# Kernel tuning notes

Measured on AMD Instinct MI355X. Metric: run time of the kernel, lower is better.

The kernel has to match this reference:

```python
import jax, jax.numpy as jnp
import numpy as np
from functools import partial

DN = ('NHWC', 'HWIO', 'NHWC')

def conv2d(x, w, stride=1, padding='SAME'):
    return jax.lax.conv_general_dilated(x, w, (stride, stride), padding, dimension_numbers=DN)

def hard_sigmoid(x):
    return jnp.clip(0.2 * x + 0.5, 0.0, 1.0)

def leaky_relu(x):
    return jnp.where(x >= 0, x, 0.3 * x)  # Keras LeakyReLU default alpha=0.3

def conv_lstm2d(inp, wx, wh, b):
    # inp: [B,T,H,W,Cin]; returns last hidden state h: [B,H,W,1]
    B, T, H, W, _ = inp.shape
    nf = wh.shape[2]  # filters = 1
    x_t_first = jnp.transpose(inp, (1, 0, 2, 3, 4))  # [T,B,H,W,Cin]
    h0 = jnp.zeros((B, H, W, nf), inp.dtype)
    c0 = jnp.zeros((B, H, W, nf), inp.dtype)

    def step(carry, x_t):
        h, c = carry
        z = conv2d(x_t, wx) + conv2d(h, wh) + b  # [B,H,W,4*nf]
        zi, zf, zc, zo = jnp.split(z, 4, axis=-1)  # Keras gate order i,f,c,o
        i = hard_sigmoid(zi)
        f = hard_sigmoid(zf)
        c_new = f * c + i * jnp.tanh(zc)
        o = hard_sigmoid(zo)
        h_new = o * jnp.tanh(c_new)
        return (h_new, c_new), None

    (h_last, _), _ = jax.lax.scan(step, (h0, c0), x_t_first)
    return h_last

def setup_inputs() -> dict:
    key = jax.random.key(0)
    ks = jax.random.split(key, 16)
    s = 0.05  # small init scale (mimics 0.02 normal init)
    d = {
        'inp': jax.random.normal(ks[0], (64, 24, 82, 67, 6), jnp.float32),
        'tar': jax.random.normal(ks[1], (64, 82, 67, 5), jnp.float32),
        'wx': jax.random.normal(ks[2], (3, 3, 6, 4), jnp.float32) * s,
        'wh': jax.random.normal(ks[3], (3, 3, 1, 4), jnp.float32) * s,
        'b_lstm': jnp.zeros((4,), jnp.float32),
        'w1': jax.random.normal(ks[4], (5, 5, 6, 64), jnp.float32) * s,
        'b1': jnp.zeros((64,), jnp.float32),
        'w2': jax.random.normal(ks[5], (5, 5, 64, 128), jnp.float32) * s,
        'b2': jnp.zeros((128,), jnp.float32),
        'w3': jax.random.normal(ks[6], (4, 4, 128, 512), jnp.float32) * s,
        'bn_gamma': jnp.ones((512,), jnp.float32),
        'bn_beta': jnp.zeros((512,), jnp.float32),
        'bn_mean': jnp.zeros((512,), jnp.float32),
        'bn_var': jax.random.uniform(ks[7], (512,), jnp.float32, 0.5, 1.5),
        'w4': jax.random.normal(ks[8], (4, 4, 512, 1), jnp.float32) * s,
        'b4': jnp.zeros((1,), jnp.float32),
    }
    return d

def reference(inp, tar, wx, wh, b_lstm, w1, b1, w2, b2, w3,
              bn_gamma, bn_beta, bn_mean, bn_var, w4, b4):
    # ConvLSTM2D(1, 3, same, return_sequences=False)
    h = conv_lstm2d(inp, wx, wh, b_lstm)          # [B,82,67,1]
    x = jnp.concatenate([h, tar], axis=-1)        # [B,82,67,6]
    # Conv2D(64,5,s2,same) + LeakyReLU (+ Dropout: identity at inference)
    x = leaky_relu(conv2d(x, w1, 2, 'SAME') + b1)  # [B,41,34,64]
    # Conv2D(128,5,s2,same) + LeakyReLU
    x = leaky_relu(conv2d(x, w2, 2, 'SAME') + b2)  # [B,21,17,128]
    # ZeroPadding2D
    x = jnp.pad(x, ((0, 0), (1, 1), (1, 1), (0, 0)))  # [B,23,19,128]
    # Conv2D(512,4,s1,valid,no bias)
    x = conv2d(x, w3, 1, 'VALID')                  # [B,20,16,512]
    # BatchNormalization (inference, eps=1e-3 Keras default)
    x = (x - bn_mean) * jax.lax.rsqrt(bn_var + 1e-3) * bn_gamma + bn_beta
    x = leaky_relu(x)
    x = jnp.pad(x, ((0, 0), (1, 1), (1, 1), (0, 0)))  # [B,22,18,512]
    # Conv2D(1,4,s1,valid)
    x = conv2d(x, w4, 1, 'VALID') + b4             # [B,19,15,1]
    return x
```

## Files before the change

### kernel.cpp

```cpp
#include <hip/hip_runtime.h>
#include <hip/hip_bf16.h>
#include <cstdint>

#define DEV static __device__ __forceinline__

typedef __attribute__((ext_vector_type(8))) short short8;
typedef __attribute__((ext_vector_type(4))) float f32x4;
typedef __attribute__((ext_vector_type(2))) float f32x2;

DEV uint32_t bf16rne(float f) {
    uint32_t u = __float_as_uint(f);
    uint32_t r = u + 0x7FFFu + ((u >> 16) & 1u);
    return r >> 16;
}
DEV float bf16tof(uint32_t h) { return __uint_as_float((h & 0xFFFFu) << 16); }
DEV float hsig(float z) { return fminf(fmaxf(0.2f * z + 0.5f, 0.f), 1.f); }
DEV float lrelu(float x) { return x >= 0.f ? x : 0.3f * x; }
DEV float ftanh(float x) {
    float e = __expf(2.0f * x);
    return 1.0f - 2.0f * __builtin_amdgcn_rcpf(e + 1.0f);
}

DEV void gload16(const void* g, void* l) {
    __builtin_amdgcn_global_load_lds(
        reinterpret_cast<const __attribute__((address_space(1))) uint32_t*>(
            reinterpret_cast<uintptr_t>(g)),
        reinterpret_cast<__attribute__((address_space(3))) uint32_t*>(
            reinterpret_cast<uintptr_t>(l)),
        16, 0, 0);
}

#define HH 82
#define WW 67
#define PIX (HH * WW)
#define BB 64
#define TT 24

#define NXZ 8442
#define NPREP 512

__global__ __launch_bounds__(256) void k_xz(
    const float* __restrict__ inp, const float* __restrict__ wx,
    const float* __restrict__ bl, uint2* __restrict__ xz,
    const float* __restrict__ w1, const float* __restrict__ w2,
    const float* __restrict__ w3,
    ushort* __restrict__ w1t, ushort* __restrict__ w2t, ushort* __restrict__ w3t,
    uint4* __restrict__ z1, uint4* __restrict__ z2, uint4* __restrict__ z3)
{
    if (blockIdx.x >= NXZ) {
        const int Z1 = 852480, Z2 = 447488;
        const int W2 = 204800, W3 = 1048576, W1 = 12288, Z3 = 32;
        const int total = Z1 + Z2 + W2 + W3 + W1 + Z3;
        for (int id = (blockIdx.x - NXZ) * 256 + threadIdx.x; id < total;
             id += NPREP * 256) {
            if (id < Z1) {
                z1[id] = make_uint4(0, 0, 0, 0);
            } else if (id < Z1 + Z2) {
                z2[id - Z1] = make_uint4(0, 0, 0, 0);
            } else if (id < Z1 + Z2 + W2) {
                int idx = id - (Z1 + Z2);
                int n = idx / 1600, k = idx - n * 1600;
                w2t[idx] = (ushort)bf16rne(w2[(size_t)k * 128 + n]);
            } else if (id < Z1 + Z2 + W2 + W3) {
                int idx = id - (Z1 + Z2 + W2);
                int n = idx >> 11, k = idx & 2047;
                w3t[idx] = (ushort)bf16rne(w3[(size_t)k * 512 + n]);
            } else if (id < Z1 + Z2 + W2 + W3 + W1) {
                int idx = id - (Z1 + Z2 + W2 + W3);
                int n = idx / 192, k = idx % 192;
                w1t[idx] = (k < 150) ? (ushort)bf16rne(w1[(size_t)k * 64 + n])
                                     : (ushort)0;
            } else {
                z3[id - (Z1 + Z2 + W2 + W3 + W1)] = make_uint4(0, 0, 0, 0);
            }
        }
        return;
    }

    const int id = blockIdx.x * 256 + threadIdx.x;
    const int x  = id % 67;
    const int g  = (id / 67) % 21;
    const int bt = id / (67 * 21);
    if (bt >= BB * TT) return;
    const int y0 = g * 4;
    const float* img = inp + (size_t)bt * (PIX * 6);

    f32x2 a01[4], a23[4];
    const f32x2 bias01 = {bl[0], bl[1]};
    const f32x2 bias23 = {bl[2], bl[3]};
    #pragma unroll
    for (int o = 0; o < 4; ++o) { a01[o] = bias01; a23[o] = bias23; }

    #pragma unroll
    for (int rr = 0; rr < 6; ++rr) {
        const int iy = y0 - 1 + rr;
        if (iy < 0 || iy >= HH) continue;

        f32x2 vf[9];
        #pragma unroll
        for (int q = 0; q < 9; ++q) vf[q] = (f32x2){0.f, 0.f};
        const float* rp = img + (size_t)iy * 402 + (x - 1) * 6;
        if (x > 0) {
            vf[0] = *(const f32x2*)(rp);
            vf[1] = *(const f32x2*)(rp + 2);
            vf[2] = *(const f32x2*)(rp + 4);
        }
        vf[3] = *(const f32x2*)(rp + 6);
        vf[4] = *(const f32x2*)(rp + 8);
        vf[5] = *(const f32x2*)(rp + 10);
        if (x < 66) {
            vf[6] = *(const f32x2*)(rp + 12);
            vf[7] = *(const f32x2*)(rp + 14);
            vf[8] = *(const f32x2*)(rp + 16);
        }

        #pragma unroll
        for (int o = 0; o < 4; ++o) {
            const int dy = rr - o;
            if (dy < 0 || dy > 2) continue;
            #pragma unroll
            for (int kx = 0; kx < 3; ++kx) {
                const float* w6 = wx + (dy * 3 + kx) * 24;
                #pragma unroll
                for (int ci = 0; ci < 6; ++ci) {
                    const f32x2 w01 = *(const f32x2*)(w6 + ci * 4);
                    const f32x2 w23 = *(const f32x2*)(w6 + ci * 4 + 2);
                    const int fi = kx * 6 + ci;
                    const float s = vf[fi >> 1][fi & 1];
                    a01[o] += s * w01;
                    a23[o] += s * w23;
                }
            }
        }
    }

    #pragma unroll
    for (int o = 0; o < 4; ++o) {
        const int y = y0 + o;
        if (y < HH) {
            uint32_t lo = bf16rne(a01[o][0]) | (bf16rne(a01[o][1]) << 16);
            uint32_t hi = bf16rne(a23[o][0]) | (bf16rne(a23[o][1]) << 16);
            xz[((size_t)bt * HH + y) * WW + x] = make_uint2(lo, hi);
        }
    }
}

#define HPB 41
#define LROWS 42
__global__ __launch_bounds__(1024) void k_lstm(
    const uint2* __restrict__ xz, const float* __restrict__ wh,
    float* __restrict__ hout, int* __restrict__ gxi, int* __restrict__ flags)
{
    __shared__ float hb[2][LROWS * WW];
    __shared__ uint2 xt[2][2748];
    const int bid = blockIdx.x;
    const int b = bid >> 1, h = bid & 1;
    const int tid = threadIdx.x;

    float whr[9][4];
    #pragma unroll
    for (int k = 0; k < 9; ++k)
        #pragma unroll
        for (int g = 0; g < 4; ++g) whr[k][g] = wh[k * 4 + g];

    for (int i = tid; i < LROWS * WW; i += 1024) { hb[0][i] = 0.f; }

    const bool active = tid < 943;
    const int r  = active ? tid / 23 : 0;
    const int gr = h * HPB + r;
    const int lr = r + (h ? 1 : 0);
    const int x0 = (tid % 23) * 3;
    const int len = active ? ((x0 + 3 <= WW) ? 3 : (WW - x0)) : 0;
    const bool isb = active && ((h == 0 && r == 40) || (h == 1 && r == 0));
    float c[3];
    #pragma unroll
    for (int j = 0; j < 3; ++j) c[j] = 0.f;

    const int base_px = h ? 2746 : 0;
    const char* xzb = (const char*)xz + (((size_t)b * TT) * PIX + base_px) * 8;
    int* myflag = flags + bid;
    int* nbflag = flags + (bid ^ 1);
    const int gx_my = ((b * 2 + h) * 2) * 68;
    const int gx_nb = ((b * 2 + (h ^ 1)) * 2) * 68;

    #pragma unroll
    for (int k = 0; k < 2; ++k) {
        int idx = tid + k * 1024;
        if (idx < 1374)
            gload16(xzb + (size_t)idx * 16, (char*)xt[0] + (size_t)idx * 16);
    }
    __syncthreads();

    int cur = 0;
    #pragma unroll 1
    for (int t = 0; t < TT; ++t) {
        const int nxt = cur ^ 1;
        const int par = (t + 1) & 1;
        if (t < TT - 1) {
            const char* srcn = xzb + (size_t)(t + 1) * (PIX * 8);
            #pragma unroll
            for (int k = 0; k < 2; ++k) {
                int idx = tid + k * 1024;
                if (idx < 1374)
                    gload16(srcn + (size_t)idx * 16,
                            (char*)xt[nxt] + (size_t)idx * 16);
            }
        }
        if (active) {
            float z[3][4];
            #pragma unroll
            for (int j = 0; j < 3; ++j) {
                int xi = x0 + j; if (xi > WW - 1) xi = WW - 1;
                uint2 zp = xt[cur][gr * WW + xi - base_px];
                z[j][0] = bf16tof(zp.x); z[j][1] = bf16tof(zp.x >> 16);
                z[j][2] = bf16tof(zp.y); z[j][3] = bf16tof(zp.y >> 16);
            }
            #pragma unroll
            for (int ky = 0; ky < 3; ++ky) {
                int giy = gr + ky - 1;
                if (giy < 0 || giy >= HH) continue;
                const float* hr = &hb[cur][(giy - (h ? 40 : 0)) * WW];
                #pragma unroll
                for (int dx = -1; dx < 4; ++dx) {
                    int xi = x0 + dx;
                    if (xi < 0 || xi >= WW) continue;
                    float hv = hr[xi];
                    #pragma unroll
                    for (int kx = 0; kx < 3; ++kx) {
                        int xo = dx - kx + 1;
                        if (xo < 0 || xo > 2) continue;
                        #pragma unroll
                        for (int g = 0; g < 4; ++g)
                            z[xo][g] = fmaf(hv, whr[ky * 3 + kx][g], z[xo][g]);
                    }
                }
            }
            float* hw = &hb[nxt][lr * WW];
            #pragma unroll
            for (int j = 0; j < 3; ++j) {
                float fi = hsig(z[j][0]), ff = hsig(z[j][1]), fo = hsig(z[j][3]);
                float cn = ff * c[j] + fi * ftanh(z[j][2]);
                c[j] = cn;
                if (j < len) {
                    float hv = fo * ftanh(cn);
                    hw[x0 + j] = hv;
                    if (isb)
                        atomicExch(&gxi[gx_my + par * 68 + x0 + j],
                                   __float_as_int(hv));
                }
            }
        }
        __syncthreads();
        if (tid == 0) {
            atomicExch(myflag, t + 1);
            while (atomicAdd(nbflag, 0) < t + 1) { __builtin_amdgcn_s_sleep(8); }
        }
        __syncthreads();
        if (tid < WW) {
            int v = atomicAdd(&gxi[gx_nb + par * 68 + tid], 0);
            hb[nxt][(h ? 0 : 41) * WW + tid] = __int_as_float(v);
        }
        __syncthreads();
        cur = nxt;
    }
    float* ho = hout + (size_t)b * PIX + (size_t)h * 2747;
    const float* src = hb[cur] + (h ? WW : 0);
    for (int i = tid; i < 2747; i += 1024)
        ho[i] = src[i];
}

__global__ __launch_bounds__(256) void k_im2col(
    const float* __restrict__ hin, const float* __restrict__ tar,
    uint* __restrict__ A1)
{
    const int id = blockIdx.x * 256 + threadIdx.x;
    const int p = id % 28;
    const int m = id / 28;
    if (m >= 89216) return;
    uint* dst = A1 + (size_t)m * 96;
    if (p >= 25) {
        uint* q = dst + 75 + (p - 25) * 7;
        #pragma unroll
        for (int i = 0; i < 7; ++i) q[i] = 0;
        return;
    }
    const int x = m % 34;
    const int y = (m / 34) % 41;
    const int b = m / 1394;
    const int ky = p / 5, kx = p % 5;
    const int iy = 2 * y + ky - 1;
    const int ix = 2 * x + kx - 2;
    float v[6] = {0.f, 0.f, 0.f, 0.f, 0.f, 0.f};
    if (iy >= 0 && iy < HH && ix >= 0 && ix < WW) {
        const int pi = b * PIX + iy * WW + ix;
        v[0] = hin[pi];
        const float* tp = tar + (size_t)pi * 5;
        #pragma unroll
        for (int c = 0; c < 5; ++c) v[c + 1] = tp[c];
    }
    uint* q = dst + p * 3;
    q[0] = bf16rne(v[0]) | (bf16rne(v[1]) << 16);
    q[1] = bf16rne(v[2]) | (bf16rne(v[3]) << 16);
    q[2] = bf16rne(v[4]) | (bf16rne(v[5]) << 16);
}

__global__ __launch_bounds__(256) void k_gemm1(
    const ushort* __restrict__ A1, const ushort* __restrict__ w1t,
    const float* __restrict__ b1, ushort* __restrict__ x1p)
{
    constexpr int M = 89216;
    __shared__ ushort At[256 * 64];
    __shared__ ushort Bl[64 * 64];

    const int tid = threadIdx.x;
    const int wid = tid >> 6, lane = tid & 63;
    const int m0 = blockIdx.x * 256;
    const int swz = (((lane & 7) ^ ((lane >> 3) & 7)) << 3);

    int arow[8], brow[2];
    #pragma unroll
    for (int i = 0; i < 8; ++i) {
        int row = wid * 64 + i * 8 + (lane >> 3);
        int m = m0 + row; if (m > M - 1) m = M - 1;
        arow[i] = m * 192;
    }
    #pragma unroll
    for (int i = 0; i < 2; ++i) {
        int row = wid * 16 + i * 8 + (lane >> 3);
        brow[i] = row * 192;
    }

    f32x4 acc[4][4];
    #pragma unroll
    for (int i = 0; i < 4; ++i)
        #pragma unroll
        for (int j = 0; j < 4; ++j) acc[i][j] = (f32x4){0.f, 0.f, 0.f, 0.f};

    #pragma unroll 1
    for (int kp = 0; kp < 3; ++kp) {
        const int koff = kp * 64;
        #pragma unroll
        for (int i = 0; i < 8; ++i)
            gload16(A1 + arow[i] + koff + swz,
                    (void*)(At + (wid * 64 + i * 8) * 64));
        #pragma unroll
        for (int i = 0; i < 2; ++i)
            gload16(w1t + brow[i] + koff + swz,
                    (void*)(Bl + (wid * 16 + i * 8) * 64));
        __syncthreads();
        #pragma unroll
        for (int ks = 0; ks < 2; ++ks) {
            short8 af[4], bf[4];
            const int lc = ks * 64 + ((lane >> 4) << 4);
            #pragma unroll
            for (int mf = 0; mf < 4; ++mf) {
                int row = wid * 64 + mf * 16 + (lane & 15);
                af[mf] = *(const short8*)((const char*)At + row * 128 + (lc ^ ((row & 7) << 4)));
            }
            #pragma unroll
            for (int nf = 0; nf < 4; ++nf) {
                int row = nf * 16 + (lane & 15);
                bf[nf] = *(const short8*)((const char*)Bl + row * 128 + (lc ^ ((row & 7) << 4)));
            }
            #pragma unroll
            for (int mf = 0; mf < 4; ++mf)
                #pragma unroll
                for (int nf = 0; nf < 4; ++nf)
                    acc[mf][nf] = __builtin_amdgcn_mfma_f32_16x16x32_bf16(
                        af[mf], bf[nf], acc[mf][nf], 0, 0, 0);
        }
        __syncthreads();
    }

    #pragma unroll
    for (int nf = 0; nf < 4; ++nf) {
        int n = nf * 16 + (lane & 15);
        float bias = b1[n];
        #pragma unroll
        for (int mf = 0; mf < 4; ++mf) {
            int mbase = m0 + wid * 64 + mf * 16 + ((lane >> 4) << 2);
            #pragma unroll
            for (int r = 0; r < 4; ++r) {
                int m = mbase + r;
                if (m < M) {
                    int x = m % 34, y = (m / 34) % 41, b = m / 1394;
                    float v = lrelu(acc[mf][nf][r] + bias);
                    x1p[((size_t)(b * 45 + y + 2) * 37 + (x + 1)) * 64 + n] =
                        (ushort)bf16rne(v);
                }
            }
        }
    }
}

template<bool IS3>
__global__ __launch_bounds__(256) void k_convm(
    const ushort* __restrict__ Ain, const ushort* __restrict__ Bt,
    const float* __restrict__ p0, const float* __restrict__ p1,
    const float* __restrict__ p2, const float* __restrict__ p3,
    ushort* __restrict__ outp)
{
    constexpr int OH = IS3 ? 20 : 21, OW = IS3 ? 16 : 17;
    constexpr int PH = IS3 ? 23 : 45, PW = IS3 ? 19 : 37;
    constexpr int CIN = IS3 ? 128 : 64;
    constexpr int KW_ = IS3 ? 4 : 5;
    constexpr int KK  = IS3 ? 16 : 25;
    constexpr int STR = IS3 ? 1 : 2;
    constexpr int HALVES = CIN / 64;
    constexpr int MPB = OH * OW;
    constexpr int M = 64 * MPB;
    constexpr int KTOT = KK * CIN;

    __shared__ ushort At[128 * 64];
    __shared__ ushort Bl[64 * 64];

    const int tid = threadIdx.x;
    const int wid = tid >> 6, lane = tid & 63;
    const int m0 = blockIdx.x * 128;
    const int n0 = blockIdx.y * 64;
    const int wr = wid >> 1, wc = wid & 1;

    const int swz = (((lane & 7) ^ ((lane >> 3) & 7)) << 3);

    int arow_base[4], brow_base[2];
    #pragma unroll
    for (int i = 0; i < 4; ++i) {
        int row = wid * 32 + i * 8 + (lane >> 3);
        int m = m0 + row; if (m > M - 1) m = M - 1;
        int b = m / MPB, r = m % MPB;
        int y = r / OW, x = r % OW;
        arow_base[i] = ((b * PH + y * STR) * PW + x * STR) * CIN;
    }
    #pragma unroll
    for (int i = 0; i < 2; ++i) {
        int row = wid * 16 + i * 8 + (lane >> 3);
        brow_base[i] = (n0 + row) * KTOT;
    }

    f32x4 acc[4][2];
    #pragma unroll
    for (int i = 0; i < 4; ++i)
        #pragma unroll
        for (int j = 0; j < 2; ++j) acc[i][j] = (f32x4){0.f, 0.f, 0.f, 0.f};

    #pragma unroll 1
    for (int kp = 0; kp < KK; ++kp) {
        const int ky = kp / KW_, kx = kp % KW_;
        const int aoff = (ky * PW + kx) * CIN;
        #pragma unroll
        for (int h = 0; h < HALVES; ++h) {
            const int koff = h * 64;
            #pragma unroll
            for (int i = 0; i < 4; ++i)
                gload16(Ain + arow_base[i] + aoff + koff + swz,
                        (void*)(At + (wid * 32 + i * 8) * 64));
            #pragma unroll
            for (int i = 0; i < 2; ++i)
                gload16(Bt + brow_base[i] + kp * CIN + koff + swz,
                        (void*)(Bl + (wid * 16 + i * 8) * 64));
            __syncthreads();
            #pragma unroll
            for (int ks = 0; ks < 2; ++ks) {
                short8 af[4], bf[2];
                const int lc = ks * 64 + ((lane >> 4) << 4);
                #pragma unroll
                for (int mf = 0; mf < 4; ++mf) {
                    int row = wr * 64 + mf * 16 + (lane & 15);
                    af[mf] = *(const short8*)((const char*)At + row * 128 + (lc ^ ((row & 7) << 4)));
                }
                #pragma unroll
                for (int nf = 0; nf < 2; ++nf) {
                    int row = wc * 32 + nf * 16 + (lane & 15);
                    bf[nf] = *(const short8*)((const char*)Bl + row * 128 + (lc ^ ((row & 7) << 4)));
                }
                #pragma unroll
                for (int mf = 0; mf < 4; ++mf)
                    #pragma unroll
                    for (int nf = 0; nf < 2; ++nf)
                        acc[mf][nf] = __builtin_amdgcn_mfma_f32_16x16x32_bf16(
                            af[mf], bf[nf], acc[mf][nf], 0, 0, 0);
            }
            __syncthreads();
        }
    }

    if (IS3) {
        #pragma unroll
        for (int nf = 0; nf < 2; ++nf) {
            int n = n0 + wc * 32 + nf * 16 + (lane & 15);
            float sc = p0[n] * rsqrtf(p3[n] + 1e-3f);
            float sh = p1[n] - p2[n] * sc;
            #pragma unroll
            for (int mf = 0; mf < 4; ++mf) {
                int mbase = m0 + wr * 64 + mf * 16 + ((lane >> 4) << 2);
                #pragma unroll
                for (int r = 0; r < 4; ++r) {
                    float v = lrelu(acc[mf][nf][r] * sc + sh);
                    outp[(size_t)(mbase + r) * 512 + n] = (ushort)bf16rne(v);
                }
            }
        }
    } else {
        #pragma unroll
        for (int nf = 0; nf < 2; ++nf) {
            int n = n0 + wc * 32 + nf * 16 + (lane & 15);
            float bias = p0[n];
            #pragma unroll
            for (int mf = 0; mf < 4; ++mf) {
                int mbase = m0 + wr * 64 + mf * 16 + ((lane >> 4) << 2);
                #pragma unroll
                for (int r = 0; r < 4; ++r) {
                    int m = mbase + r;
                    if (m < M) {
                        int b = m / MPB, rr = m % MPB;
                        int y = rr / OW, x = rr % OW;
                        float v = lrelu(acc[mf][nf][r] + bias);
                        outp[((size_t)((b * 23) + (y + 1)) * 19 + (x + 1)) * 128 + n] =
                            (ushort)bf16rne(v);
                    }
                }
            }
        }
    }
}

__global__ __launch_bounds__(256) void k_conv4(
    const ushort* __restrict__ x3, const float* __restrict__ w4,
    const float* __restrict__ b4, float* __restrict__ out)
{
    __shared__ float red[4][16];
    const int b = blockIdx.x / 19, y = blockIdx.x % 19;
    const int wid = threadIdx.x >> 6, lane = threadIdx.x & 63;
    const int c0 = lane * 8;
    float acc[15];
    #pragma unroll
    for (int x = 0; x < 15; ++x) acc[x] = 0.f;
    #pragma unroll 1
    for (int ky = 0; ky < 4; ++ky) {
        int iy = y + ky - 1;
        if (iy < 0 || iy >= 20) continue;
        float w[4][8];
        #pragma unroll
        for (int kx = 0; kx < 4; ++kx) {
            const float4 wa = *(const float4*)(w4 + (ky * 4 + kx) * 512 + c0);
            const float4 wb = *(const float4*)(w4 + (ky * 4 + kx) * 512 + c0 + 4);
            w[kx][0] = wa.x; w[kx][1] = wa.y; w[kx][2] = wa.z; w[kx][3] = wa.w;
            w[kx][4] = wb.x; w[kx][5] = wb.y; w[kx][6] = wb.z; w[kx][7] = wb.w;
        }
        #pragma unroll
        for (int ixl = 0; ixl < 4; ++ixl) {
            const int ix = wid * 4 + ixl;
            uint4 u = *(const uint4*)(x3 + ((size_t)(b * 20 + iy) * 16 + ix) * 512 + c0);
            float v[8];
            v[0] = bf16tof(u.x); v[1] = bf16tof(u.x >> 16);
            v[2] = bf16tof(u.y); v[3] = bf16tof(u.y >> 16);
            v[4] = bf16tof(u.z); v[5] = bf16tof(u.z >> 16);
            v[6] = bf16tof(u.w); v[7] = bf16tof(u.w >> 16);
            #pragma unroll
            for (int kx = 0; kx < 4; ++kx) {
                int x = ix - kx + 1;
                if (x < 0 || x > 14) continue;
                float s = 0.f;
                #pragma unroll
                for (int c = 0; c < 8; ++c) s = fmaf(v[c], w[kx][c], s);
                acc[x] += s;
            }
        }
    }
    #pragma unroll
    for (int x = 0; x < 15; ++x) {
        float s = acc[x];
        #pragma unroll
        for (int off = 32; off > 0; off >>= 1)
            s += __shfl_down(s, off);
        if (lane == 0) red[wid][x] = s;
    }
    __syncthreads();
    if (threadIdx.x < 15) {
        float s = red[0][threadIdx.x] + red[1][threadIdx.x] +
                  red[2][threadIdx.x] + red[3][threadIdx.x] + b4[0];
        out[(size_t)blockIdx.x * 15 + threadIdx.x] = s;
    }
}

extern "C" void kernel_launch(void* const* d_in, const int* in_sizes, int n_in,
                              void* d_out, int out_size, void* d_ws, size_t ws_size,
                              hipStream_t stream)
{
    const float* inp  = (const float*)d_in[0];
    const float* tar  = (const float*)d_in[1];
    const float* wx   = (const float*)d_in[2];
    const float* wh   = (const float*)d_in[3];
    const float* bl   = (const float*)d_in[4];
    const float* w1   = (const float*)d_in[5];
    const float* b1   = (const float*)d_in[6];
    const float* w2   = (const float*)d_in[7];
    const float* b2   = (const float*)d_in[8];
    const float* w3   = (const float*)d_in[9];
    const float* gam  = (const float*)d_in[10];
    const float* bet  = (const float*)d_in[11];
    const float* mean = (const float*)d_in[12];
    const float* var  = (const float*)d_in[13];
    const float* w4   = (const float*)d_in[14];
    const float* b4   = (const float*)d_in[15];
    float* out = (float*)d_out;

    char* ws = (char*)d_ws;
    uint2*  xz    = (uint2*)(ws);
    ushort* A1    = (ushort*)(ws);
    ushort* x3b   = (ushort*)(ws);
    float*  hfin  = (float*)(ws + 67510272);
    ushort* x1p   = (ushort*)(ws + 68916736);
    ushort* x2p   = (ushort*)(ws + 82556416);
    ushort* w2t   = (ushort*)(ws + 89716224);
    ushort* w3t   = (ushort*)(ws + 90125824);
    ushort* w1t   = (ushort*)(ws + 92222976);
    int*    gxi   = (int*)(ws + 92247552);
    int*    flags = (int*)(ws + 92386816);

    k_xz<<<NXZ + NPREP, 256, 0, stream>>>(inp, wx, bl, xz,
                                          w1, w2, w3, w1t, w2t, w3t,
                                          (uint4*)x1p, (uint4*)x2p, (uint4*)flags);
    k_lstm<<<BB * 2, 1024, 0, stream>>>(xz, wh, hfin, gxi, flags);

    k_im2col<<<(89216 * 28 + 255) / 256, 256, 0, stream>>>(hfin, tar, (uint*)A1);
    k_gemm1<<<349, 256, 0, stream>>>(A1, w1t, b1, x1p);

    dim3 g2(179, 2);
    k_convm<false><<<g2, 256, 0, stream>>>(x1p, w2t, b2, nullptr, nullptr, nullptr, x2p);
    dim3 g3(160, 8);
    k_convm<true><<<g3, 256, 0, stream>>>(x2p, w3t, gam, bet, mean, var, x3b);

    k_conv4<<<BB * 19, 256, 0, stream>>>(x3b, w4, b4, out);
}
```

Baseline: 325.9 us.

## Split ConvLSTM recurrence into four row-band blocks per batch with halo exchange

The recurrent LSTM kernel moves from 2 blocks of 1024 threads per batch image to 4 blocks of 512 threads, each owning about 21 rows. Each block now trades top and bottom halo rows with up to two neighbours through global atomics and flag spin-waits, and the flag and halo buffers are enlarged to match. The aim is more concurrent blocks across the GPU's compute units and a shorter per-step critical path. In exchange each timestep needs more inter-block synchronisation and halo traffic, and the spin-waits depend on all blocks being co-resident.

```diff
diff --git a/kernel.cpp b/kernel.cpp
--- a/kernel.cpp
+++ b/kernel.cpp
@@ -49,7 +49,7 @@
 {
     if (blockIdx.x >= NXZ) {
         const int Z1 = 852480, Z2 = 447488;
-        const int W2 = 204800, W3 = 1048576, W1 = 12288, Z3 = 32;
+        const int W2 = 204800, W3 = 1048576, W1 = 12288, Z3 = 64;
         const int total = Z1 + Z2 + W2 + W3 + W1 + Z3;
         for (int id = (blockIdx.x - NXZ) * 256 + threadIdx.x; id < total;
              id += NPREP * 256) {
@@ -145,16 +145,16 @@
     }
 }
 
-#define HPB 41
-#define LROWS 42
-__global__ __launch_bounds__(1024) void k_lstm(
+__global__ __launch_bounds__(512) void k_lstm(
     const uint2* __restrict__ xz, const float* __restrict__ wh,
     float* __restrict__ hout, int* __restrict__ gxi, int* __restrict__ flags)
 {
-    __shared__ float hb[2][LROWS * WW];
-    __shared__ uint2 xt[2][2748];
+    __shared__ float hb[2][23 * WW];
+    __shared__ uint2 xt[2][1408];
     const int bid = blockIdx.x;
-    const int b = bid >> 1, h = bid & 1;
+    const int b = bid >> 2, qb = bid & 3;
+    const int r0 = qb * 21;
+    const int nrows = (qb == 3) ? 19 : 21;
     const int tid = threadIdx.x;
 
     float whr[9][4];
@@ -163,30 +163,31 @@
         #pragma unroll
         for (int g = 0; g < 4; ++g) whr[k][g] = wh[k * 4 + g];
 
-    for (int i = tid; i < LROWS * WW; i += 1024) { hb[0][i] = 0.f; }
-
-    const bool active = tid < 943;
+    for (int i = tid; i < 23 * WW; i += 512) hb[0][i] = 0.f;
+
+    const bool active = tid < nrows * 23;
     const int r  = active ? tid / 23 : 0;
-    const int gr = h * HPB + r;
-    const int lr = r + (h ? 1 : 0);
+    const int gr = r0 + r;
+    const int lr = r + 1;
     const int x0 = (tid % 23) * 3;
     const int len = active ? ((x0 + 3 <= WW) ? 3 : (WW - x0)) : 0;
-    const bool isb = active && ((h == 0 && r == 40) || (h == 1 && r == 0));
+    const bool wr_top = active && (r == 0) && (qb > 0);
+    const bool wr_bot = active && (r == nrows - 1) && (qb < 3);
     float c[3];
     #pragma unroll
     for (int j = 0; j < 3; ++j) c[j] = 0.f;
 
-    const int base_px = h ? 2746 : 0;
+    const int base_px = (r0 * WW) & ~1;
+    const int end_px = (r0 + nrows) * WW;
+    const int nch = (end_px - base_px + 1) >> 1;
     const char* xzb = (const char*)xz + (((size_t)b * TT) * PIX + base_px) * 8;
     int* myflag = flags + bid;
-    int* nbflag = flags + (bid ^ 1);
-    const int gx_my = ((b * 2 + h) * 2) * 68;
-    const int gx_nb = ((b * 2 + (h ^ 1)) * 2) * 68;
+    #define GX(bb, par, side) (((((bb) * 2) + (par)) * 2 + (side)) * 68)
 
     #pragma unroll
     for (int k = 0; k < 2; ++k) {
-        int idx = tid + k * 1024;
-        if (idx < 1374)
+        int idx = tid + k * 512;
+        if (idx < nch)
             gload16(xzb + (size_t)idx * 16, (char*)xt[0] + (size_t)idx * 16);
     }
     __syncthreads();
@@ -200,8 +201,8 @@
             const char* srcn = xzb + (size_t)(t + 1) * (PIX * 8);
             #pragma unroll
             for (int k = 0; k < 2; ++k) {
-                int idx = tid + k * 1024;
-                if (idx < 1374)
+                int idx = tid + k * 512;
+                if (idx < nch)
                     gload16(srcn + (size_t)idx * 16,
                             (char*)xt[nxt] + (size_t)idx * 16);
             }
@@ -219,7 +220,7 @@
             for (int ky = 0; ky < 3; ++ky) {
                 int giy = gr + ky - 1;
                 if (giy < 0 || giy >= HH) continue;
-                const float* hr = &hb[cur][(giy - (h ? 40 : 0)) * WW];
+                const float* hr = &hb[cur][(giy - r0 + 1) * WW];
                 #pragma unroll
                 for (int dx = -1; dx < 4; ++dx) {
                     int xi = x0 + dx;
@@ -244,8 +245,11 @@
                 if (j < len) {
                     float hv = fo * ftanh(cn);
                     hw[x0 + j] = hv;
-                    if (isb)
-                        atomicExch(&gxi[gx_my + par * 68 + x0 + j],
+                    if (wr_top)
+                        atomicExch(&gxi[GX(bid, par, 0) + x0 + j],
+                                   __float_as_int(hv));
+                    if (wr_bot)
+                        atomicExch(&gxi[GX(bid, par, 1) + x0 + j],
                                    __float_as_int(hv));
                 }
             }
@@ -253,19 +257,28 @@
         __syncthreads();
         if (tid == 0) {
             atomicExch(myflag, t + 1);
-            while (atomicAdd(nbflag, 0) < t + 1) { __builtin_amdgcn_s_sleep(8); }
+            if (qb > 0)
+                while (atomicAdd(flags + bid - 1, 0) < t + 1) { __builtin_amdgcn_s_sleep(8); }
+            if (qb < 3)
+                while (atomicAdd(flags + bid + 1, 0) < t + 1) { __builtin_amdgcn_s_sleep(8); }
         }
         __syncthreads();
         if (tid < WW) {
-            int v = atomicAdd(&gxi[gx_nb + par * 68 + tid], 0);
-            hb[nxt][(h ? 0 : 41) * WW + tid] = __int_as_float(v);
+            if (qb > 0) {
+                int v = atomicAdd(&gxi[GX(bid - 1, par, 1) + tid], 0);
+                hb[nxt][tid] = __int_as_float(v);
+            }
+            if (qb < 3) {
+                int v = atomicAdd(&gxi[GX(bid + 1, par, 0) + tid], 0);
+                hb[nxt][(nrows + 1) * WW + tid] = __int_as_float(v);
+            }
         }
         __syncthreads();
         cur = nxt;
     }
-    float* ho = hout + (size_t)b * PIX + (size_t)h * 2747;
-    const float* src = hb[cur] + (h ? WW : 0);
-    for (int i = tid; i < 2747; i += 1024)
+    float* ho = hout + (size_t)b * PIX + (size_t)(r0 * WW);
+    const float* src = hb[cur] + WW;
+    for (int i = tid; i < nrows * WW; i += 512)
         ho[i] = src[i];
 }
 
@@ -616,12 +629,12 @@
     ushort* w3t   = (ushort*)(ws + 90125824);
     ushort* w1t   = (ushort*)(ws + 92222976);
     int*    gxi   = (int*)(ws + 92247552);
-    int*    flags = (int*)(ws + 92386816);
+    int*    flags = (int*)(ws + 92526080);
 
     k_xz<<<NXZ + NPREP, 256, 0, stream>>>(inp, wx, bl, xz,
                                           w1, w2, w3, w1t, w2t, w3t,
                                           (uint4*)x1p, (uint4*)x2p, (uint4*)flags);
-    k_lstm<<<BB * 2, 1024, 0, stream>>>(xz, wh, hfin, gxi, flags);
+    k_lstm<<<BB * 4, 512, 0, stream>>>(xz, wh, hfin, gxi, flags);
 
     k_im2col<<<(89216 * 28 + 255) / 256, 256, 0, stream>>>(hfin, tar, (uint*)A1);
     k_gemm1<<<349, 256, 0, stream>>>(A1, w1t, b1, x1p);
```

Measured after the change: 340.1 us. 4.4% more time.
